# Optimization experiments

Measured on AMD Instinct MI355X. Metric: run time of the kernel, lower is better.

Reference implementation:

```python
import jax, jax.numpy as jnp
import numpy as np

NUM_HEADS = 16
HIDDEN = 1152
MLP = 4304
HEAD_DIM = HIDDEN // NUM_HEADS  # 72
SEQ = 3072
LN_EPS = 1e-5


def setup_inputs() -> dict:
    key = jax.random.key(0)
    ks = jax.random.split(key, 16)
    inv = 1.0 / np.sqrt(HIDDEN)
    inv_m = 1.0 / np.sqrt(MLP)
    pos = jnp.arange(SEQ, dtype=jnp.float32)[:, None]
    freq = jnp.exp(-jnp.arange(HEAD_DIM // 2, dtype=jnp.float32) * (np.log(10000.0) / (HEAD_DIM // 2)))
    ang = pos * freq[None, :]
    return {
        "hidden_states": jax.random.normal(ks[0], (SEQ, HIDDEN), jnp.float32),
        "rope_cos": jnp.cos(ang),
        "rope_sin": jnp.sin(ang),
        "ln0_g": jnp.ones((HIDDEN,), jnp.float32),
        "ln0_b": jnp.zeros((HIDDEN,), jnp.float32),
        "ln1_g": jnp.ones((HIDDEN,), jnp.float32),
        "ln1_b": jnp.zeros((HIDDEN,), jnp.float32),
        "wqkv_w": jax.random.normal(ks[1], (3 * HIDDEN, HIDDEN), jnp.float32) * inv,
        "wqkv_b": jnp.zeros((3 * HIDDEN,), jnp.float32),
        "wo_w": jax.random.normal(ks[2], (HIDDEN, HIDDEN), jnp.float32) * inv,
        "wo_b": jnp.zeros((HIDDEN,), jnp.float32),
        "fc0_w": jax.random.normal(ks[3], (MLP, HIDDEN), jnp.float32) * inv,
        "fc0_b": jnp.zeros((MLP,), jnp.float32),
        "fc1_w": jax.random.normal(ks[4], (HIDDEN, MLP), jnp.float32) * inv_m,
        "fc1_b": jnp.zeros((HIDDEN,), jnp.float32),
    }


def _layernorm(x, g, b):
    mu = jnp.mean(x, axis=-1, keepdims=True)
    var = jnp.mean(jnp.square(x - mu), axis=-1, keepdims=True)
    return (x - mu) * jax.lax.rsqrt(var + LN_EPS) * g + b


def _apply_rope(x, cos, sin):
    # x: [S, H, Dh]; cos/sin: [S, Dh/2]
    xp = x.astype(jnp.float32).reshape(*x.shape[:-1], -1, 2)  # [S, H, Dh/2, 2]
    xr, xi = xp[..., 0], xp[..., 1]
    c = cos[:, None, :]
    s = sin[:, None, :]
    out_r = xr * c - xi * s
    out_i = xr * s + xi * c
    return jnp.stack([out_r, out_i], axis=-1).reshape(x.shape).astype(x.dtype)


def reference(hidden_states, rope_cos, rope_sin, ln0_g, ln0_b, ln1_g, ln1_b,
              wqkv_w, wqkv_b, wo_w, wo_b, fc0_w, fc0_b, fc1_w, fc1_b):
    S = hidden_states.shape[0]
    residual = hidden_states
    h = _layernorm(hidden_states, ln0_g, ln0_b)
    xqkv = (h @ wqkv_w.T + wqkv_b).reshape(S, 3, NUM_HEADS, HEAD_DIM)
    xq, xk, xv = xqkv[:, 0], xqkv[:, 1], xqkv[:, 2]
    xq = _apply_rope(xq, rope_cos, rope_sin)
    xk = _apply_rope(xk, rope_cos, rope_sin)
    scale = 1.0 / np.sqrt(HEAD_DIM)
    scores = jnp.einsum('shd,thd->hst', xq, xk) * scale  # [H, S, S]
    attn = jax.nn.softmax(scores.astype(jnp.float32), axis=-1).astype(xq.dtype)
    out = jnp.einsum('hst,thd->shd', attn, xv).reshape(S, HIDDEN)
    h = residual + (out @ wo_w.T + wo_b)
    residual = h
    h = _layernorm(h, ln1_g, ln1_b)
    h = jax.nn.gelu(h @ fc0_w.T + fc0_b, approximate=True)
    h = h @ fc1_w.T + fc1_b
    return residual + h
```

## Files before the change

kernel.cpp:

```cpp
#include <hip/hip_runtime.h>
#include <hip/hip_bf16.h>
#include <math.h>

typedef __hip_bfloat16 bf16;
typedef __attribute__((ext_vector_type(8))) short short8;
typedef __attribute__((ext_vector_type(4))) short short4v;
typedef __attribute__((ext_vector_type(4))) float f32x4;

#define SEQ 3072
#define HID 1152
#define NHEAD 16
#define HD 72
#define HDP 96
#define MLPD 4304
#define MLPP 4352

__device__ __forceinline__ void async_lds16(void* lds, const void* g) {
  __builtin_amdgcn_global_load_lds((const __attribute__((address_space(1))) void*)g,
                                   (__attribute__((address_space(3))) void*)lds,
                                   16, 0, 0);
}

__device__ __forceinline__ short bf16b(float x) {
  __hip_bfloat16 h = __float2bfloat16(x);
  return *reinterpret_cast<short*>(&h);
}

__device__ __forceinline__ unsigned cvt_pk2(float a, float b) {
  unsigned r;
  asm("v_cvt_pk_bf16_f32 %0, %1, %2" : "=v"(r) : "v"(a), "v"(b));
  return r;
}

__global__ __launch_bounds__(256) void cast_bf16_k(const float* __restrict__ in,
                                                   unsigned* __restrict__ out2, int n4) {
  int stride = gridDim.x * blockDim.x;
  for (int i = blockIdx.x * blockDim.x + threadIdx.x; i < n4; i += stride) {
    float4 u = ((const float4*)in)[i];
    uint2 w = make_uint2(cvt_pk2(u.x, u.y), cvt_pk2(u.z, u.w));
    ((uint2*)out2)[i] = w;
  }
}

__global__ __launch_bounds__(256) void cast_pad_rows_k(const float* __restrict__ in,
                                                       unsigned* __restrict__ out2,
                                                       int R, int C4, int n4) {
  int stride = gridDim.x * blockDim.x;
  for (int i = blockIdx.x * blockDim.x + threadIdx.x; i < n4; i += stride) {
    int r = i / C4;
    uint2 w = make_uint2(0u, 0u);
    if (r < R) {
      float4 u = ((const float4*)in)[i];
      w = make_uint2(cvt_pk2(u.x, u.y), cvt_pk2(u.z, u.w));
    }
    ((uint2*)out2)[i] = w;
  }
}

__global__ __launch_bounds__(256) void cast_pad_cols_k(const float* __restrict__ in,
                                                       unsigned* __restrict__ out2,
                                                       int C4, int Cp4, int n4) {
  int stride = gridDim.x * blockDim.x;
  for (int i = blockIdx.x * blockDim.x + threadIdx.x; i < n4; i += stride) {
    int r = i / Cp4, c4 = i - r * Cp4;
    uint2 w = make_uint2(0u, 0u);
    if (c4 < C4) {
      float4 u = ((const float4*)in)[r * C4 + c4];
      w = make_uint2(cvt_pk2(u.x, u.y), cvt_pk2(u.z, u.w));
    }
    ((uint2*)out2)[i] = w;
  }
}

__global__ __launch_bounds__(256) void ln_k(const float* __restrict__ x,
                                            const float* __restrict__ g,
                                            const float* __restrict__ b,
                                            bf16* __restrict__ o) {
  int row = blockIdx.x;
  const float4* xr = (const float4*)(x + (size_t)row * HID);
  float sum = 0.f, sq = 0.f;
  for (int c = threadIdx.x; c < HID / 4; c += 256) {
    float4 u = xr[c];
    sum += u.x + u.y + u.z + u.w;
    sq += u.x * u.x + u.y * u.y + u.z * u.z + u.w * u.w;
  }
#pragma unroll
  for (int off = 32; off > 0; off >>= 1) {
    sum += __shfl_down(sum, off, 64);
    sq += __shfl_down(sq, off, 64);
  }
  __shared__ float red[8];
  int wv = threadIdx.x >> 6;
  if ((threadIdx.x & 63) == 0) { red[wv] = sum; red[4 + wv] = sq; }
  __syncthreads();
  if (threadIdx.x == 0) {
    red[0] = red[0] + red[1] + red[2] + red[3];
    red[4] = red[4] + red[5] + red[6] + red[7];
  }
  __syncthreads();
  float mu = red[0] * (1.f / HID);
  float var = red[4] * (1.f / HID) - mu * mu;
  float inv = rsqrtf(var + 1e-5f);
  uint2* o4 = (uint2*)(o + (size_t)row * HID);
  const float4* g4 = (const float4*)g;
  const float4* b4 = (const float4*)b;
  for (int c = threadIdx.x; c < HID / 4; c += 256) {
    float4 u = xr[c], gg = g4[c], bb = b4[c];
    uint2 w = make_uint2(cvt_pk2((u.x - mu) * inv * gg.x + bb.x, (u.y - mu) * inv * gg.y + bb.y),
                         cvt_pk2((u.z - mu) * inv * gg.z + bb.z, (u.w - mu) * inv * gg.w + bb.w));
    o4[c] = w;
  }
}

template <int EPI>
__global__ __launch_bounds__(256) void gemm_bf16(const bf16* __restrict__ A,
                                                 const bf16* __restrict__ Bt,
                                                 const float* __restrict__ bias, int nbias,
                                                 const float* __restrict__ res,
                                                 float* __restrict__ outf,
                                                 bf16* __restrict__ outb,
                                                 int M, int N, int K) {
  __shared__ bf16 As[3][128 * 32];
  __shared__ bf16 Bs[3][128 * 32];
  const int t = threadIdx.x;
  const int l = t & 63;
  const int w = t >> 6;
  const int wr = w >> 1, wc = w & 1;
  const int lrow = l & 15;
  const int lk = (l >> 4) * 8;
  const int m0 = blockIdx.y * 128;
  const int n0 = blockIdx.x * 128;
  const int arow = t >> 2;
  const int ach = (t & 3) * 8;

  const bf16* pa0 = &A[(size_t)(m0 + arow) * K + ach];
  const bf16* pa1 = &A[(size_t)(m0 + arow + 64) * K + ach];
  const bf16* pb0 = &Bt[(size_t)(n0 + arow) * K + ach];
  const bf16* pb1 = &Bt[(size_t)(n0 + arow + 64) * K + ach];
  auto STAGE = [&](int buf, int kt) {
    size_t off = (size_t)kt * 32;
    async_lds16(&As[buf][t * 8], pa0 + off);
    async_lds16(&As[buf][(256 + t) * 8], pa1 + off);
    async_lds16(&Bs[buf][t * 8], pb0 + off);
    async_lds16(&Bs[buf][(256 + t) * 8], pb1 + off);
  };

  f32x4 acc[4][4] = {};
  const int nkt = K >> 5;
  STAGE(0, 0);
  STAGE(1, 1);
  int bcur = 0;
  for (int kt = 0; kt < nkt; ++kt) {
    if (kt + 1 < nkt) {
      asm volatile("s_waitcnt vmcnt(4)" ::: "memory");
    } else {
      asm volatile("s_waitcnt vmcnt(0)" ::: "memory");
    }
    __builtin_amdgcn_s_barrier();
    int bn2 = bcur + 2;
    if (bn2 >= 3) bn2 -= 3;
    if (kt + 2 < nkt) STAGE(bn2, kt + 2);

    short8 af[4], bfr[4];
#pragma unroll
    for (int i = 0; i < 4; ++i)
      af[i] = *(const short8*)&As[bcur][(wr * 64 + i * 16 + lrow) * 32 + lk];
#pragma unroll
    for (int i = 0; i < 4; ++i)
      bfr[i] = *(const short8*)&Bs[bcur][(wc * 64 + i * 16 + lrow) * 32 + lk];
    __builtin_amdgcn_s_setprio(1);
#pragma unroll
    for (int i = 0; i < 4; ++i)
#pragma unroll
      for (int j = 0; j < 4; ++j)
        acc[i][j] = __builtin_amdgcn_mfma_f32_16x16x32_bf16(af[i], bfr[j], acc[i][j], 0, 0, 0);
    __builtin_amdgcn_s_setprio(0);
    ++bcur;
    if (bcur == 3) bcur = 0;
  }

#pragma unroll
  for (int i = 0; i < 4; ++i) {
    int rowb = m0 + wr * 64 + i * 16 + (l >> 4) * 4;
#pragma unroll
    for (int j = 0; j < 4; ++j) {
      int col = n0 + wc * 64 + j * 16 + lrow;
      float bv = (col < nbias) ? bias[col] : 0.f;
#pragma unroll
      for (int r2 = 0; r2 < 4; ++r2) {
        size_t idx = (size_t)(rowb + r2) * N + col;
        float v = acc[i][j][r2] + bv;
        if (EPI == 0) {
          outf[idx] = v;
        } else if (EPI == 1) {
          outf[idx] = v + res[idx];
        } else {
          float gel = 0.5f * v * (1.f + tanhf(0.7978845608028654f * (v + 0.044715f * v * v * v)));
          outb[idx] = __float2bfloat16(gel);
        }
      }
    }
  }
}

__global__ __launch_bounds__(256) void rope_split(const float* __restrict__ xqkv,
                                                  const float* __restrict__ cosb,
                                                  const float* __restrict__ sinb,
                                                  bf16* __restrict__ qp,
                                                  bf16* __restrict__ kp,
                                                  bf16* __restrict__ vt) {
  __shared__ bf16 vl[64][72];
  const int t = threadIdx.x;
  const int h = blockIdx.y;
  const int s0 = blockIdx.x * 64;
  const float scale = 0.11785113019775793f;
  for (int idx = t; idx < 64 * 48; idx += 256) {
    int sl = idx / 48, pi = idx - sl * 48;
    int srow = s0 + sl;
    size_t obase = ((size_t)h * SEQ + srow) * HDP + 2 * pi;
    if (pi < 36) {
      const float* xr = xqkv + (size_t)srow * (3 * HID) + h * HD + 2 * pi;
      float qr = xr[0], qi = xr[1];
      float kr = xr[HID], ki = xr[HID + 1];
      float c = cosb[srow * 36 + pi], sn = sinb[srow * 36 + pi];
      *(unsigned*)&qp[obase] = cvt_pk2((qr * c - qi * sn) * scale, (qr * sn + qi * c) * scale);
      *(unsigned*)&kp[obase] = cvt_pk2(kr * c - ki * sn, kr * sn + ki * c);
    } else {
      *(unsigned*)&qp[obase] = 0u;
      *(unsigned*)&kp[obase] = 0u;
    }
  }
  for (int idx = t; idx < 64 * 72; idx += 256) {
    int sl = idx / 72, d = idx - sl * 72;
    vl[sl][d] = __float2bfloat16(xqkv[(size_t)(s0 + sl) * (3 * HID) + 2 * HID + h * HD + d]);
  }
  __syncthreads();
  bf16 z = __float2bfloat16(0.f);
  for (int idx = t; idx < HDP * 64; idx += 256) {
    int d = idx / 64, sl = idx - d * 64;
    vt[((size_t)h * HDP + d) * SEQ + s0 + sl] = (d < 72) ? vl[sl][d] : z;
  }
}

__global__ __launch_bounds__(256) void flash_attn(const bf16* __restrict__ q,
                                                  const bf16* __restrict__ kk,
                                                  const bf16* __restrict__ vT,
                                                  bf16* __restrict__ o) {
  __shared__ alignas(16) bf16 KV3[3 * 6144];
  __shared__ alignas(16) bf16 Pl[4][512];
  const int t = threadIdx.x;
  const int l = t & 63;
  const int w = t >> 6;
  const int g = l >> 4;
  const int lrow = l & 15;
  const int bid = blockIdx.x;
  const int kq = bid >> 3;
  const int h = (bid & 7) * 2 + (kq & 1);
  const int q0 = (kq >> 1) * 64 + w * 16;
  const int NT = SEQ / 32;

  const bf16* sbase[3];
  int smul[3];
#pragma unroll
  for (int i = 0; i < 3; ++i) {
    int s = t + i * 256;
    if (s < 384) {
      int cb = s >> 5, kv = s & 31;
      sbase[i] = kk + ((size_t)h * SEQ + kv) * HDP + cb * 8;
      smul[i] = 32 * HDP;
    } else {
      int vs = s - 384;
      int cb = vs / 96, d = vs - cb * 96;
      sbase[i] = vT + ((size_t)h * HDP + d) * SEQ + cb * 8;
      smul[i] = 32;
    }
  }
  auto STAGE = [&](int tile, int bufOff) {
#pragma unroll
    for (int i = 0; i < 3; ++i)
      async_lds16(&KV3[bufOff + (t + i * 256) * 8], sbase[i] + (size_t)tile * smul[i]);
  };

  short8 qf[3];
#pragma unroll
  for (int f = 0; f < 3; ++f)
    qf[f] = *(const short8*)&q[((size_t)h * SEQ + q0 + lrow) * HDP + f * 32 + g * 8];

  float m_r = -1e30f, l_r = 0.f;
  f32x4 oa[5] = {};

  STAGE(0, 0);
  STAGE(1, 6144);
  STAGE(2, 12288);
  asm volatile("s_waitcnt vmcnt(6)" ::: "memory");
  __builtin_amdgcn_s_barrier();

  f32x4 stA[2] = {}, stB[2];
  int b0 = 0;
#pragma unroll
  for (int nf = 0; nf < 2; ++nf)
#pragma unroll
    for (int f = 0; f < 3; ++f) {
      short8 kfrag = *(const short8*)&KV3[0 + (f * 4 + g) * 256 + (nf * 16 + lrow) * 8];
      stA[nf] = __builtin_amdgcn_mfma_f32_16x16x32_bf16(kfrag, qf[f], stA[nf], 0, 0, 0);
    }

  for (int kt = 0; kt < NT - 1; ++kt) {
    int b1 = b0 + 6144;
    if (b1 == 18432) b1 = 0;
    asm volatile("s_waitcnt vmcnt(3)" ::: "memory");
    __builtin_amdgcn_s_barrier();

    stB[0] = (f32x4){0.f, 0.f, 0.f, 0.f};
    stB[1] = (f32x4){0.f, 0.f, 0.f, 0.f};
    __builtin_amdgcn_s_setprio(1);
#pragma unroll
    for (int nf = 0; nf < 2; ++nf)
#pragma unroll
      for (int f = 0; f < 3; ++f) {
        short8 kfrag = *(const short8*)&KV3[b1 + (f * 4 + g) * 256 + (nf * 16 + lrow) * 8];
        stB[nf] = __builtin_amdgcn_mfma_f32_16x16x32_bf16(kfrag, qf[f], stB[nf], 0, 0, 0);
      }
    __builtin_amdgcn_s_setprio(0);

    float pmax = fmaxf(fmaxf(fmaxf(stA[0][0], stA[0][1]), fmaxf(stA[0][2], stA[0][3])),
                       fmaxf(fmaxf(stA[1][0], stA[1][1]), fmaxf(stA[1][2], stA[1][3])));
    if (!__all(pmax - m_r <= 8.f)) {
      float rm = pmax;
      rm = fmaxf(rm, __shfl_xor(rm, 16, 64));
      rm = fmaxf(rm, __shfl_xor(rm, 32, 64));
      float mn = fmaxf(m_r, rm);
      float alpha = __expf(m_r - mn);
      l_r *= alpha;
#pragma unroll
      for (int nf = 0; nf < 5; ++nf)
#pragma unroll
        for (int r = 0; r < 4; ++r) oa[nf][r] *= alpha;
      m_r = mn;
    }
#pragma unroll
    for (int nf = 0; nf < 2; ++nf)
#pragma unroll
      for (int r = 0; r < 4; ++r) stA[nf][r] = __expf(stA[nf][r] - m_r);
    l_r += (stA[0][0] + stA[0][1]) + (stA[0][2] + stA[0][3]) +
           (stA[1][0] + stA[1][1]) + (stA[1][2] + stA[1][3]);

#pragma unroll
    for (int nf = 0; nf < 2; ++nf) {
      uint2* dst = (uint2*)&Pl[w][(2 * nf + (g >> 1)) * 128 + lrow * 8 + (g & 1) * 4];
      *dst = make_uint2(cvt_pk2(stA[nf][0], stA[nf][1]), cvt_pk2(stA[nf][2], stA[nf][3]));
    }

    {
      short8 pa = *(const short8*)&Pl[w][g * 128 + lrow * 8];
      __builtin_amdgcn_s_setprio(1);
#pragma unroll
      for (int nf = 0; nf < 5; ++nf) {
        short8 bv = *(const short8*)&KV3[b0 + 3072 + g * 768 + (nf * 16 + lrow) * 8];
        oa[nf] = __builtin_amdgcn_mfma_f32_16x16x32_bf16(bv, pa, oa[nf], 0, 0, 0);
      }
      __builtin_amdgcn_s_setprio(0);
    }

    asm volatile("s_waitcnt lgkmcnt(0)" ::: "memory");
    __builtin_amdgcn_s_barrier();
    int s = kt + 3;
    if (s >= NT) s -= NT;
    STAGE(s, b0);
    stA[0] = stB[0];
    stA[1] = stB[1];
    b0 = b1;
  }

  {
    float pmax = fmaxf(fmaxf(fmaxf(stA[0][0], stA[0][1]), fmaxf(stA[0][2], stA[0][3])),
                       fmaxf(fmaxf(stA[1][0], stA[1][1]), fmaxf(stA[1][2], stA[1][3])));
    if (!__all(pmax - m_r <= 8.f)) {
      float rm = pmax;
      rm = fmaxf(rm, __shfl_xor(rm, 16, 64));
      rm = fmaxf(rm, __shfl_xor(rm, 32, 64));
      float mn = fmaxf(m_r, rm);
      float alpha = __expf(m_r - mn);
      l_r *= alpha;
#pragma unroll
      for (int nf = 0; nf < 5; ++nf)
#pragma unroll
        for (int r = 0; r < 4; ++r) oa[nf][r] *= alpha;
      m_r = mn;
    }
#pragma unroll
    for (int nf = 0; nf < 2; ++nf)
#pragma unroll
      for (int r = 0; r < 4; ++r) stA[nf][r] = __expf(stA[nf][r] - m_r);
    l_r += (stA[0][0] + stA[0][1]) + (stA[0][2] + stA[0][3]) +
           (stA[1][0] + stA[1][1]) + (stA[1][2] + stA[1][3]);
#pragma unroll
    for (int nf = 0; nf < 2; ++nf) {
      uint2* dst = (uint2*)&Pl[w][(2 * nf + (g >> 1)) * 128 + lrow * 8 + (g & 1) * 4];
      *dst = make_uint2(cvt_pk2(stA[nf][0], stA[nf][1]), cvt_pk2(stA[nf][2], stA[nf][3]));
    }
    short8 pa = *(const short8*)&Pl[w][g * 128 + lrow * 8];
#pragma unroll
    for (int nf = 0; nf < 5; ++nf) {
      short8 bv = *(const short8*)&KV3[b0 + 3072 + g * 768 + (nf * 16 + lrow) * 8];
      oa[nf] = __builtin_amdgcn_mfma_f32_16x16x32_bf16(bv, pa, oa[nf], 0, 0, 0);
    }
  }

  float lt = l_r;
  lt += __shfl_xor(lt, 16, 64);
  lt += __shfl_xor(lt, 32, 64);
  float rcp = 1.f / lt;
  size_t obase = (size_t)(q0 + lrow) * HID + h * HD;
#pragma unroll
  for (int nf = 0; nf < 5; ++nf) {
    int d = nf * 16 + g * 4;
    if (d + 3 < HD) {
      uint2 pk = make_uint2(cvt_pk2(oa[nf][0] * rcp, oa[nf][1] * rcp),
                            cvt_pk2(oa[nf][2] * rcp, oa[nf][3] * rcp));
      *(uint2*)&o[obase + d] = pk;
    }
  }
}

extern "C" void kernel_launch(void* const* d_in, const int* in_sizes, int n_in,
                              void* d_out, int out_size, void* d_ws, size_t ws_size,
                              hipStream_t stream) {
  (void)in_sizes; (void)n_in; (void)out_size;
  const float* hidden = (const float*)d_in[0];
  const float* cosb = (const float*)d_in[1];
  const float* sinb = (const float*)d_in[2];
  const float* ln0g = (const float*)d_in[3];
  const float* ln0b = (const float*)d_in[4];
  const float* ln1g = (const float*)d_in[5];
  const float* ln1b = (const float*)d_in[6];
  const float* wqkv = (const float*)d_in[7];
  const float* bqkv = (const float*)d_in[8];
  const float* wo = (const float*)d_in[9];
  const float* bo = (const float*)d_in[10];
  const float* w0 = (const float*)d_in[11];
  const float* b0 = (const float*)d_in[12];
  const float* w1 = (const float*)d_in[13];
  const float* b1 = (const float*)d_in[14];

  char* p = (char*)d_ws;
  auto alloc = [&](size_t n) {
    char* r = p;
    p += (n + 255) & ~(size_t)255;
    return r;
  };
  bf16* wqkv_bf = (bf16*)alloc((size_t)3 * HID * HID * 2);
  bf16* wo_bf = (bf16*)alloc((size_t)HID * HID * 2);
  bf16* fc0_bf = (bf16*)alloc((size_t)MLPP * HID * 2);
  bf16* fc1_bf = (bf16*)alloc((size_t)HID * MLPP * 2);
  bf16* ln0_bf = (bf16*)alloc((size_t)SEQ * HID * 2);
  float* xqkv = (float*)alloc((size_t)SEQ * 3 * HID * 4);
  bf16* qp = (bf16*)alloc((size_t)NHEAD * SEQ * HDP * 2);
  bf16* kp = (bf16*)alloc((size_t)NHEAD * SEQ * HDP * 2);
  bf16* vt = (bf16*)alloc((size_t)NHEAD * HDP * SEQ * 2);
  bf16* attn_bf = (bf16*)alloc((size_t)SEQ * HID * 2);
  float* h1 = (float*)alloc((size_t)SEQ * HID * 4);
  bf16* ln1_bf = (bf16*)alloc((size_t)SEQ * HID * 2);
  bf16* gelu_bf = (bf16*)alloc((size_t)SEQ * MLPP * 2);
  if ((size_t)(p - (char*)d_ws) > ws_size) return;

  dim3 blk(256);
  cast_bf16_k<<<2048, blk, 0, stream>>>(wqkv, (unsigned*)wqkv_bf, 3 * HID * HID / 4);
  cast_bf16_k<<<1024, blk, 0, stream>>>(wo, (unsigned*)wo_bf, HID * HID / 4);
  cast_pad_rows_k<<<2048, blk, 0, stream>>>(w0, (unsigned*)fc0_bf, MLPD, HID / 4, MLPP * HID / 4);
  cast_pad_cols_k<<<2048, blk, 0, stream>>>(w1, (unsigned*)fc1_bf, MLPD / 4, MLPP / 4, HID * MLPP / 4);
  ln_k<<<SEQ, blk, 0, stream>>>(hidden, ln0g, ln0b, ln0_bf);
  gemm_bf16<0><<<dim3(3 * HID / 128, SEQ / 128), blk, 0, stream>>>(
      ln0_bf, wqkv_bf, bqkv, 3 * HID, nullptr, xqkv, nullptr, SEQ, 3 * HID, HID);
  rope_split<<<dim3(SEQ / 64, NHEAD), blk, 0, stream>>>(xqkv, cosb, sinb, qp, kp, vt);
  flash_attn<<<dim3(768), blk, 0, stream>>>(qp, kp, vt, attn_bf);
  gemm_bf16<1><<<dim3(HID / 128, SEQ / 128), blk, 0, stream>>>(
      attn_bf, wo_bf, bo, HID, hidden, h1, nullptr, SEQ, HID, HID);
  ln_k<<<SEQ, blk, 0, stream>>>(h1, ln1g, ln1b, ln1_bf);
  gemm_bf16<2><<<dim3(MLPP / 128, SEQ / 128), blk, 0, stream>>>(
      ln1_bf, fc0_bf, b0, MLPD, nullptr, nullptr, gelu_bf, SEQ, MLPP, HID);
  gemm_bf16<1><<<dim3(HID / 128, SEQ / 128), blk, 0, stream>>>(
      gelu_bf, fc1_bf, b1, HID, h1, (float*)d_out, nullptr, SEQ, HID, MLPP);
}
```

Before: 401.1 us.

## Remap GEMM tiles across XCDs, use exp2 softmax, cheaper GELU

GEMM launches become 1D grids, and each block index is remapped so that consecutive tiles land on the same XCD (blockIdx&7 striding), with M-tiles walked inside each N column. The goal is better L2 reuse of weight tiles. Softmax moves to base 2: log2(e) is folded into the Q scale, the raw v_exp_f32 instruction is used, and the rescale threshold is widened to match. The tanh-GELU is rewritten as v·sigmoid(2u) using __expf with clamping, which avoids tanhf. The exp2 change carries a small precision risk.

```diff
diff --git a/kernel.cpp b/kernel.cpp
--- a/kernel.cpp
+++ b/kernel.cpp
@@ -21,14 +21,15 @@
                                    16, 0, 0);
 }
 
-__device__ __forceinline__ short bf16b(float x) {
-  __hip_bfloat16 h = __float2bfloat16(x);
-  return *reinterpret_cast<short*>(&h);
-}
-
 __device__ __forceinline__ unsigned cvt_pk2(float a, float b) {
   unsigned r;
   asm("v_cvt_pk_bf16_f32 %0, %1, %2" : "=v"(r) : "v"(a), "v"(b));
+  return r;
+}
+
+__device__ __forceinline__ float exp2a(float x) {
+  float r;
+  asm("v_exp_f32 %0, %1" : "=v"(r) : "v"(x));
   return r;
 }
 
@@ -128,8 +129,12 @@
   const int wr = w >> 1, wc = w & 1;
   const int lrow = l & 15;
   const int lk = (l >> 4) * 8;
-  const int m0 = blockIdx.y * 128;
-  const int n0 = blockIdx.x * 128;
+  const int wg = (blockIdx.x & 7) * (gridDim.x >> 3) + (blockIdx.x >> 3);
+  const int gyt = M >> 7;
+  const int xt = wg / gyt;
+  const int yt = wg - xt * gyt;
+  const int m0 = yt * 128;
+  const int n0 = xt * 128;
   const int arow = t >> 2;
   const int ach = (t & 3) * 8;
 
@@ -195,8 +200,10 @@
         } else if (EPI == 1) {
           outf[idx] = v + res[idx];
         } else {
-          float gel = 0.5f * v * (1.f + tanhf(0.7978845608028654f * (v + 0.044715f * v * v * v)));
-          outb[idx] = __float2bfloat16(gel);
+          float u = 0.7978845608028654f * (v + 0.044715f * v * v * v);
+          u = fminf(fmaxf(u, -15.f), 15.f);
+          float tt = __expf(2.f * u);
+          outb[idx] = __float2bfloat16(v * tt / (tt + 1.f));
         }
       }
     }
@@ -213,7 +220,7 @@
   const int t = threadIdx.x;
   const int h = blockIdx.y;
   const int s0 = blockIdx.x * 64;
-  const float scale = 0.11785113019775793f;
+  const float scale = 0.17002445f;
   for (int idx = t; idx < 64 * 48; idx += 256) {
     int sl = idx / 48, pi = idx - sl * 48;
     int srow = s0 + sl;
@@ -325,12 +332,12 @@
 
     float pmax = fmaxf(fmaxf(fmaxf(stA[0][0], stA[0][1]), fmaxf(stA[0][2], stA[0][3])),
                        fmaxf(fmaxf(stA[1][0], stA[1][1]), fmaxf(stA[1][2], stA[1][3])));
-    if (!__all(pmax - m_r <= 8.f)) {
+    if (!__all(pmax - m_r <= 11.54f)) {
       float rm = pmax;
       rm = fmaxf(rm, __shfl_xor(rm, 16, 64));
       rm = fmaxf(rm, __shfl_xor(rm, 32, 64));
       float mn = fmaxf(m_r, rm);
-      float alpha = __expf(m_r - mn);
+      float alpha = exp2a(m_r - mn);
       l_r *= alpha;
 #pragma unroll
       for (int nf = 0; nf < 5; ++nf)
@@ -341,7 +348,7 @@
 #pragma unroll
     for (int nf = 0; nf < 2; ++nf)
 #pragma unroll
-      for (int r = 0; r < 4; ++r) stA[nf][r] = __expf(stA[nf][r] - m_r);
+      for (int r = 0; r < 4; ++r) stA[nf][r] = exp2a(stA[nf][r] - m_r);
     l_r += (stA[0][0] + stA[0][1]) + (stA[0][2] + stA[0][3]) +
            (stA[1][0] + stA[1][1]) + (stA[1][2] + stA[1][3]);
 
@@ -375,12 +382,12 @@
   {
     float pmax = fmaxf(fmaxf(fmaxf(stA[0][0], stA[0][1]), fmaxf(stA[0][2], stA[0][3])),
                        fmaxf(fmaxf(stA[1][0], stA[1][1]), fmaxf(stA[1][2], stA[1][3])));
-    if (!__all(pmax - m_r <= 8.f)) {
+    if (!__all(pmax - m_r <= 11.54f)) {
       float rm = pmax;
       rm = fmaxf(rm, __shfl_xor(rm, 16, 64));
       rm = fmaxf(rm, __shfl_xor(rm, 32, 64));
       float mn = fmaxf(m_r, rm);
-      float alpha = __expf(m_r - mn);
+      float alpha = exp2a(m_r - mn);
       l_r *= alpha;
 #pragma unroll
       for (int nf = 0; nf < 5; ++nf)
@@ -391,7 +398,7 @@
 #pragma unroll
     for (int nf = 0; nf < 2; ++nf)
 #pragma unroll
-      for (int r = 0; r < 4; ++r) stA[nf][r] = __expf(stA[nf][r] - m_r);
+      for (int r = 0; r < 4; ++r) stA[nf][r] = exp2a(stA[nf][r] - m_r);
     l_r += (stA[0][0] + stA[0][1]) + (stA[0][2] + stA[0][3]) +
            (stA[1][0] + stA[1][1]) + (stA[1][2] + stA[1][3]);
 #pragma unroll
@@ -470,15 +477,15 @@
   cast_pad_rows_k<<<2048, blk, 0, stream>>>(w0, (unsigned*)fc0_bf, MLPD, HID / 4, MLPP * HID / 4);
   cast_pad_cols_k<<<2048, blk, 0, stream>>>(w1, (unsigned*)fc1_bf, MLPD / 4, MLPP / 4, HID * MLPP / 4);
   ln_k<<<SEQ, blk, 0, stream>>>(hidden, ln0g, ln0b, ln0_bf);
-  gemm_bf16<0><<<dim3(3 * HID / 128, SEQ / 128), blk, 0, stream>>>(
+  gemm_bf16<0><<<dim3((3 * HID / 128) * (SEQ / 128)), blk, 0, stream>>>(
       ln0_bf, wqkv_bf, bqkv, 3 * HID, nullptr, xqkv, nullptr, SEQ, 3 * HID, HID);
   rope_split<<<dim3(SEQ / 64, NHEAD), blk, 0, stream>>>(xqkv, cosb, sinb, qp, kp, vt);
   flash_attn<<<dim3(768), blk, 0, stream>>>(qp, kp, vt, attn_bf);
-  gemm_bf16<1><<<dim3(HID / 128, SEQ / 128), blk, 0, stream>>>(
+  gemm_bf16<1><<<dim3((HID / 128) * (SEQ / 128)), blk, 0, stream>>>(
       attn_bf, wo_bf, bo, HID, hidden, h1, nullptr, SEQ, HID, HID);
   ln_k<<<SEQ, blk, 0, stream>>>(h1, ln1g, ln1b, ln1_bf);
-  gemm_bf16<2><<<dim3(MLPP / 128, SEQ / 128), blk, 0, stream>>>(
+  gemm_bf16<2><<<dim3((MLPP / 128) * (SEQ / 128)), blk, 0, stream>>>(
       ln1_bf, fc0_bf, b0, MLPD, nullptr, nullptr, gelu_bf, SEQ, MLPP, HID);
-  gemm_bf16<1><<<dim3(HID / 128, SEQ / 128), blk, 0, stream>>>(
+  gemm_bf16<1><<<dim3((HID / 128) * (SEQ / 128)), blk, 0, stream>>>(
       gelu_bf, fc1_bf, b1, HID, h1, (float*)d_out, nullptr, SEQ, HID, MLPP);
 }
```

Result: faster. 380.5 us, median of 2 (-5.1%).
